# Optimization experiments

Hardware: AMD Instinct MI355X
Metric: run time of the kernel (lower is better)

The kernel has to match this reference:

```python
import jax, jax.numpy as jnp
import numpy as np

EMBED_DIM = 1024
NUM_HEADS = 16
HEAD_DIM = EMBED_DIM // NUM_HEADS
B, N = 4, 2048


def setup_inputs() -> dict:
    key = jax.random.key(0)
    k = jax.random.split(key, 5)
    s = 1.0 / np.sqrt(EMBED_DIM)
    return {
        "x": jax.random.normal(k[0], (B, N, EMBED_DIM), dtype=jnp.float32),
        "W_qkv": jax.random.uniform(k[1], (EMBED_DIM, 3 * EMBED_DIM), jnp.float32, -s, s),
        "b_qkv": jax.random.uniform(k[2], (3 * EMBED_DIM,), jnp.float32, -s, s),
        "W_proj": jax.random.uniform(k[3], (EMBED_DIM, EMBED_DIM), jnp.float32, -s, s),
        "b_proj": jax.random.uniform(k[4], (EMBED_DIM,), jnp.float32, -s, s),
    }


def reference(x, W_qkv, b_qkv, W_proj, b_proj):
    b, n, c = x.shape
    qkv = x @ W_qkv + b_qkv                       # [B,N,3C]
    qkv = qkv.reshape(b, n, 3, NUM_HEADS, HEAD_DIM)
    q = qkv[:, :, 0].transpose(0, 2, 1, 3)        # [B,H,N,D]
    k = qkv[:, :, 1].transpose(0, 2, 1, 3)
    v = qkv[:, :, 2].transpose(0, 2, 1, 3)
    scale = 1.0 / np.sqrt(HEAD_DIM).astype(np.float32)
    scores = jnp.einsum("bhqd,bhkd->bhqk", q, k) * scale
    attn = jax.nn.softmax(scores, axis=-1)
    out = jnp.einsum("bhqk,bhkd->bhqd", attn, v)  # [B,H,N,D]
    out = out.transpose(0, 2, 1, 3).reshape(b, n, c)
    return out @ W_proj + b_proj
```

## Files before the change

### kernel.cpp

```cpp
#include <hip/hip_runtime.h>
#include <math.h>


typedef __bf16 bf16x8 __attribute__((ext_vector_type(8)));
typedef float f32x4 __attribute__((ext_vector_type(4)));

#define EMBED 1024
#define NHEAD 16
#define BATCH 4
#define SEQ 2048
#define M_TOT 8192
#define QKV_N 3072
#define QSCALE 0.18033688011112042f

__device__ __forceinline__ ushort f2bf(float f) {
  union { float f; unsigned u; } x; x.f = f;
  unsigned r = x.u + 0x7FFFu + ((x.u >> 16) & 1u);
  return (ushort)(r >> 16);
}

__device__ __forceinline__ uint cvt2bf(float a, float b) {
#if __has_builtin(__builtin_amdgcn_cvt_pk_bf16_f32)
  typedef __bf16 bf16x2 __attribute__((ext_vector_type(2)));
  union { bf16x2 v; uint u; } c;
  c.v = __builtin_amdgcn_cvt_pk_bf16_f32(a, b);
  return c.u;
#else
  return (uint)f2bf(a) | ((uint)f2bf(b) << 16);
#endif
}

__device__ __forceinline__ float fexp2(float x) {
#if __has_builtin(__builtin_amdgcn_exp2f)
  return __builtin_amdgcn_exp2f(x);
#else
  return exp2f(x);
#endif
}

__device__ __forceinline__ f32x4 mfma16(bf16x8 a, bf16x8 b, f32x4 c) {
  return __builtin_amdgcn_mfma_f32_16x16x32_bf16(a, b, c, 0, 0, 0);
}

__device__ __forceinline__ void gl2lds16(const void* g, void* l) {
  __builtin_amdgcn_global_load_lds(
      (const __attribute__((address_space(1))) unsigned int*)g,
      (__attribute__((address_space(3))) unsigned int*)l, 16, 0, 0);
}

__global__ __launch_bounds__(256) void prep_kernel(
    const float* __restrict__ x, ushort* __restrict__ xb,
    const float* __restrict__ Wqkv, ushort* __restrict__ Wqkv_t,
    const float* __restrict__ Wproj, ushort* __restrict__ Wproj_t) {
  __shared__ float tile[64][65];
  const int bid = blockIdx.x;
  const int t = threadIdx.x;
  if (bid < 8192) {
    int i = (bid * 256 + t) * 4;
    float4 v = *reinterpret_cast<const float4*>(&x[i]);
    uint2 w = {cvt2bf(v.x, v.y), cvt2bf(v.z, v.w)};
    *reinterpret_cast<uint2*>(&xb[i]) = w;
    return;
  }
  const float* in;
  ushort* out;
  int Kd = 1024, Nd, n0, k0;
  if (bid < 8960) {
    int b2 = bid - 8192;
    in = Wqkv; out = Wqkv_t; Nd = 3072;
    n0 = (b2 % 48) * 64; k0 = (b2 / 48) * 64;
  } else {
    int b2 = bid - 8960;
    in = Wproj; out = Wproj_t; Nd = 1024;
    n0 = (b2 % 16) * 64; k0 = (b2 / 16) * 64;
  }
#pragma unroll
  for (int i = 0; i < 16; ++i) {
    int e = t + 256 * i;
    int kr = e >> 6, nc = e & 63;
    tile[kr][nc] = in[(size_t)(k0 + kr) * Nd + n0 + nc];
  }
  __syncthreads();
#pragma unroll
  for (int i = 0; i < 16; ++i) {
    int e = t + 256 * i;
    int nr = e >> 6, kc = e & 63;
    out[(size_t)(n0 + nr) * Kd + k0 + kc] = f2bf(tile[kc][nr]);
  }
}

__global__ __launch_bounds__(512, 4) void gemm_bf16(
    const ushort* __restrict__ A, const ushort* __restrict__ Bt,
    const float* __restrict__ bias, void* __restrict__ Cout,
    ushort* __restrict__ vtgout, int M, int N, int K, int mode) {
  __shared__ ushort As[128 * 64];
  __shared__ ushort Bs[128 * 64];
  const int t = threadIdx.x;
  const int wave = t >> 6, lane = t & 63;
  const int lane15 = lane & 15, quad = lane >> 4;
  const int m0 = blockIdx.y * 128, n0 = blockIdx.x * 128;
  const int wm = (wave >> 2) * 64, wn = (wave & 3) * 32;

  int srow[2], scol[2], sdst[2];
#pragma unroll
  for (int j = 0; j < 2; ++j) {
    int c = (j * 8 + wave) * 64 + lane;
    int row = c >> 3;
    scol[j] = ((c & 7) ^ (row & 7)) * 8;
    srow[j] = row;
    sdst[j] = (j * 8 + wave) * 512;
  }
  const int sw = lane15 & 7;

  f32x4 acc[4][2] = {};

  for (int k0 = 0; k0 < K; k0 += 64) {
#pragma unroll
    for (int j = 0; j < 2; ++j) {
      gl2lds16(&A[(size_t)(m0 + srow[j]) * K + k0 + scol[j]], &As[sdst[j]]);
      gl2lds16(&Bt[(size_t)(n0 + srow[j]) * K + k0 + scol[j]], &Bs[sdst[j]]);
    }
    __syncthreads();

#pragma unroll
    for (int kk = 0; kk < 2; ++kk) {
      bf16x8 af[4], bfr[2];
#pragma unroll
      for (int ms = 0; ms < 4; ++ms)
        af[ms] = *reinterpret_cast<const bf16x8*>(
            &As[(wm + ms * 16 + lane15) * 64 + (((kk * 4 + quad) ^ sw) * 8)]);
#pragma unroll
      for (int ns = 0; ns < 2; ++ns)
        bfr[ns] = *reinterpret_cast<const bf16x8*>(
            &Bs[(wn + ns * 16 + lane15) * 64 + (((kk * 4 + quad) ^ sw) * 8)]);
#pragma unroll
      for (int ms = 0; ms < 4; ++ms)
#pragma unroll
        for (int ns = 0; ns < 2; ++ns)
          acc[ms][ns] = mfma16(af[ms], bfr[ns], acc[ms][ns]);
    }
    __syncthreads();
  }

  if (mode == 0) {
    float* out = (float*)Cout;
#pragma unroll
    for (int ns = 0; ns < 2; ++ns) {
      int col = n0 + wn + ns * 16 + lane15;
      float bv = bias[col];
#pragma unroll
      for (int ms = 0; ms < 4; ++ms)
#pragma unroll
        for (int r = 0; r < 4; ++r) {
          int row = m0 + wm + ms * 16 + quad * 4 + r;
          out[(size_t)row * N + col] = acc[ms][ns][r] + bv;
        }
    }
  } else {
    ushort* qk = (ushort*)Cout;
#pragma unroll
    for (int ns = 0; ns < 2; ++ns) {
      int col = n0 + wn + ns * 16 + lane15;
      float bv = bias[col];
      if (col < 2048) {
        float sc = (col < 1024) ? QSCALE : 1.0f;
#pragma unroll
        for (int ms = 0; ms < 4; ++ms) {
          int row = m0 + wm + ms * 16 + quad * 4;
          uint u01 = cvt2bf((acc[ms][ns][0] + bv) * sc, (acc[ms][ns][1] + bv) * sc);
          uint u23 = cvt2bf((acc[ms][ns][2] + bv) * sc, (acc[ms][ns][3] + bv) * sc);
          qk[(size_t)(row + 0) * 2048 + col] = (ushort)u01;
          qk[(size_t)(row + 1) * 2048 + col] = (ushort)(u01 >> 16);
          qk[(size_t)(row + 2) * 2048 + col] = (ushort)u23;
          qk[(size_t)(row + 3) * 2048 + col] = (ushort)(u23 >> 16);
        }
      } else {
        int dp = col - 2048;
#pragma unroll
        for (int ms = 0; ms < 4; ++ms) {
          int row = m0 + wm + ms * 16 + quad * 4;
          int b = row >> 11, seq = row & 2047;
          uint2 w = {cvt2bf(acc[ms][ns][0] + bv, acc[ms][ns][1] + bv),
                     cvt2bf(acc[ms][ns][2] + bv, acc[ms][ns][3] + bv)};
          *reinterpret_cast<uint2*>(
              &vtgout[((size_t)(b * 1024 + dp) << 11) + seq]) = w;
        }
      }
    }
  }
}

#define QG 2

__global__ __launch_bounds__(256, 4) void attn_kernel(
    const ushort* __restrict__ qk, const ushort* __restrict__ vtg,
    ushort* __restrict__ out) {
  __shared__ ushort Ks[2][4096];
  __shared__ ushort Vt[2][4096];
  __shared__ ushort Ps[4][16 * 64];

  const int t = threadIdx.x;
  const int wave = t >> 6, lane = t & 63;
  const int lane15 = lane & 15, quad = lane >> 4;
  const int bh = blockIdx.x, qg = blockIdx.y;
  const int b = bh >> 4, h = bh & 15;
  const size_t boff = (size_t)b * SEQ * 2048;

  int sdst[2];
  const ushort* kptr[2];
  const ushort* vptr[2];
#pragma unroll
  for (int j = 0; j < 2; ++j) {
    int lg = (j * 4 + wave) * 64 + lane;
    int row = lg >> 3;
    int col = ((lg & 7) ^ (row & 7)) * 8;
    sdst[j] = (j * 4 + wave) * 512;
    kptr[j] = qk + boff + (size_t)row * 2048 + 1024 + h * 64 + col;
    vptr[j] = vtg + ((size_t)(b * 1024 + h * 64 + row) << 11) + col;
  }

  bf16x8 qf[QG][2];
#pragma unroll
  for (int g = 0; g < QG; ++g) {
    size_t qoff = boff +
        (size_t)(qg * (QG * 64) + g * 64 + wave * 16 + lane15) * 2048 + h * 64;
    qf[g][0] = *reinterpret_cast<const bf16x8*>(&qk[qoff + quad * 8]);
    qf[g][1] = *reinterpret_cast<const bf16x8*>(&qk[qoff + 32 + quad * 8]);
  }

  bf16x8 ones;
#pragma unroll
  for (int j = 0; j < 8; ++j) ones[j] = (__bf16)1.0f;

  f32x4 O[QG][4] = {};
  f32x4 lacc[QG] = {};
  const int sw = lane15 & 7;
  ushort* ps = Ps[wave];

#pragma unroll
  for (int j = 0; j < 2; ++j) {
    gl2lds16(kptr[j], &Ks[0][sdst[j]]);
    gl2lds16(vptr[j], &Vt[0][sdst[j]]);
  }
  __syncthreads();

  for (int kt = 0; kt < SEQ / 64; ++kt) {
    const int cur = kt & 1, nxt = cur ^ 1;
    if (kt < SEQ / 64 - 1) {
#pragma unroll
      for (int j = 0; j < 2; ++j) {
        gl2lds16(kptr[j] + (size_t)(kt + 1) * 64 * 2048, &Ks[nxt][sdst[j]]);
        gl2lds16(vptr[j] + (kt + 1) * 64, &Vt[nxt][sdst[j]]);
      }
    }

    bf16x8 kf[4][2], vf[2][4];
#pragma unroll
    for (int nsub = 0; nsub < 4; ++nsub) {
      const int kr = (nsub * 16 + lane15) * 64;
      kf[nsub][0] = *reinterpret_cast<const bf16x8*>(
          &Ks[cur][kr + ((quad ^ sw) * 8)]);
      kf[nsub][1] = *reinterpret_cast<const bf16x8*>(
          &Ks[cur][kr + (((quad + 4) ^ sw) * 8)]);
    }
#pragma unroll
    for (int kk = 0; kk < 2; ++kk)
#pragma unroll
      for (int dsub = 0; dsub < 4; ++dsub) {
        int d = dsub * 16 + lane15;
        vf[kk][dsub] = *reinterpret_cast<const bf16x8*>(
            &Vt[cur][d * 64 + (((kk * 4 + quad) ^ sw) * 8)]);
      }

#pragma unroll
    for (int g = 0; g < QG; ++g) {
      f32x4 st[4];
#pragma unroll
      for (int nsub = 0; nsub < 4; ++nsub) {
        f32x4 a = {-32.0f, -32.0f, -32.0f, -32.0f};
        a = mfma16(kf[nsub][0], qf[g][0], a);
        a = mfma16(kf[nsub][1], qf[g][1], a);
        st[nsub] = a;
      }
#pragma unroll
      for (int nsub = 0; nsub < 4; ++nsub) {
        uint2 w = {cvt2bf(fexp2(st[nsub][0]), fexp2(st[nsub][1])),
                   cvt2bf(fexp2(st[nsub][2]), fexp2(st[nsub][3]))};
        *reinterpret_cast<uint2*>(
            &ps[lane15 * 64 + (((2 * nsub + (quad >> 1)) ^ sw) << 3) +
                ((quad & 1) << 2)]) = w;
      }
#pragma unroll
      for (int kk = 0; kk < 2; ++kk) {
        bf16x8 pf = *reinterpret_cast<const bf16x8*>(
            &ps[lane15 * 64 + (((kk * 4 + quad) ^ sw) << 3)]);
#pragma unroll
        for (int dsub = 0; dsub < 4; ++dsub)
          O[g][dsub] = mfma16(pf, vf[kk][dsub], O[g][dsub]);
        lacc[g] = mfma16(pf, ones, lacc[g]);
      }
    }
    __syncthreads();
  }

#pragma unroll
  for (int g = 0; g < QG; ++g)
#pragma unroll
    for (int r = 0; r < 4; ++r) {
      float linv = __builtin_amdgcn_rcpf(lacc[g][r]);
      size_t rowoff =
          (size_t)(b * SEQ + qg * (QG * 64) + g * 64 + wave * 16 + quad * 4 +
                   r) * EMBED + h * 64;
      uint u01 = cvt2bf(O[g][0][r] * linv, O[g][1][r] * linv);
      uint u23 = cvt2bf(O[g][2][r] * linv, O[g][3][r] * linv);
      out[rowoff + 0 * 16 + lane15] = (ushort)u01;
      out[rowoff + 1 * 16 + lane15] = (ushort)(u01 >> 16);
      out[rowoff + 2 * 16 + lane15] = (ushort)u23;
      out[rowoff + 3 * 16 + lane15] = (ushort)(u23 >> 16);
    }
}

extern "C" void kernel_launch(void* const* d_in, const int* in_sizes, int n_in,
                              void* d_out, int out_size, void* d_ws,
                              size_t ws_size, hipStream_t stream) {
  const float* x = (const float*)d_in[0];
  const float* Wqkv = (const float*)d_in[1];
  const float* bqkv = (const float*)d_in[2];
  const float* Wproj = (const float*)d_in[3];
  const float* bproj = (const float*)d_in[4];
  float* out = (float*)d_out;

  char* ws = (char*)d_ws;
  ushort* Wqkv_t = (ushort*)ws;
  ushort* Wproj_t = (ushort*)(ws + 6291456);
  ushort* qk = (ushort*)(ws + 8388608);
  ushort* vtg = (ushort*)(ws + 41943040);
  ushort* xb = (ushort*)(ws + 58720256);
  ushort* attnout = (ushort*)(ws + 58720256);

  prep_kernel<<<8192 + 768 + 256, 256, 0, stream>>>(
      x, xb, Wqkv, Wqkv_t, Wproj, Wproj_t);
  gemm_bf16<<<dim3(QKV_N / 128, M_TOT / 128), 512, 0, stream>>>(
      xb, Wqkv_t, bqkv, qk, vtg, M_TOT, QKV_N, EMBED, 1);
  attn_kernel<<<dim3(NHEAD * BATCH, SEQ / (QG * 64)), 256, 0, stream>>>(
      qk, vtg, attnout);
  gemm_bf16<<<dim3(EMBED / 128, M_TOT / 128), 512, 0, stream>>>(
      attnout, Wproj_t, bproj, out, nullptr, M_TOT, EMBED, EMBED, 0);
}
```

Measured before the change: 284.5 us.

## Double-buffer GEMM LDS tiles with 32-wide K steps to overlap loads

Restructures the bf16 GEMM main loop to use two 128x32 LDS buffers per operand. The next K-slice is prefetched via direct global-to-LDS loads while MFMAs run on the current slice, and the XOR swizzle is adapted to the 32-element row width. This hides global load latency behind compute and keeps the LDS footprint the same. In exchange there are twice as many iterations and barriers per K, and the tighter swizzle may cause more bank conflicts.

```diff
diff --git a/kernel.cpp b/kernel.cpp
--- a/kernel.cpp
+++ b/kernel.cpp
@@ -93,52 +93,51 @@
     const ushort* __restrict__ A, const ushort* __restrict__ Bt,
     const float* __restrict__ bias, void* __restrict__ Cout,
     ushort* __restrict__ vtgout, int M, int N, int K, int mode) {
-  __shared__ ushort As[128 * 64];
-  __shared__ ushort Bs[128 * 64];
+  __shared__ ushort As[2][128 * 32];
+  __shared__ ushort Bs[2][128 * 32];
   const int t = threadIdx.x;
   const int wave = t >> 6, lane = t & 63;
   const int lane15 = lane & 15, quad = lane >> 4;
   const int m0 = blockIdx.y * 128, n0 = blockIdx.x * 128;
   const int wm = (wave >> 2) * 64, wn = (wave & 3) * 32;
 
-  int srow[2], scol[2], sdst[2];
-#pragma unroll
-  for (int j = 0; j < 2; ++j) {
-    int c = (j * 8 + wave) * 64 + lane;
-    int row = c >> 3;
-    scol[j] = ((c & 7) ^ (row & 7)) * 8;
-    srow[j] = row;
-    sdst[j] = (j * 8 + wave) * 512;
-  }
-  const int sw = lane15 & 7;
+  const int srow = t >> 2;
+  const int scol = ((t & 3) ^ ((srow >> 1) & 3)) * 8;
+  const int sdst = wave * 512;
+  const ushort* ap = &A[(size_t)(m0 + srow) * K + scol];
+  const ushort* bp = &Bt[(size_t)(n0 + srow) * K + scol];
+
+  const int sw2 = (lane15 >> 1) & 3;
 
   f32x4 acc[4][2] = {};
 
-  for (int k0 = 0; k0 < K; k0 += 64) {
-#pragma unroll
-    for (int j = 0; j < 2; ++j) {
-      gl2lds16(&A[(size_t)(m0 + srow[j]) * K + k0 + scol[j]], &As[sdst[j]]);
-      gl2lds16(&Bt[(size_t)(n0 + srow[j]) * K + k0 + scol[j]], &Bs[sdst[j]]);
-    }
-    __syncthreads();
-
-#pragma unroll
-    for (int kk = 0; kk < 2; ++kk) {
-      bf16x8 af[4], bfr[2];
-#pragma unroll
-      for (int ms = 0; ms < 4; ++ms)
-        af[ms] = *reinterpret_cast<const bf16x8*>(
-            &As[(wm + ms * 16 + lane15) * 64 + (((kk * 4 + quad) ^ sw) * 8)]);
+  const int NIT = K >> 5;
+  gl2lds16(ap, &As[0][sdst]);
+  gl2lds16(bp, &Bs[0][sdst]);
+  __syncthreads();
+
+  for (int kt = 0; kt < NIT; ++kt) {
+    const int cur = kt & 1, nxt = cur ^ 1;
+    if (kt < NIT - 1) {
+      gl2lds16(ap + (kt + 1) * 32, &As[nxt][sdst]);
+      gl2lds16(bp + (kt + 1) * 32, &Bs[nxt][sdst]);
+    }
+
+    bf16x8 af[4], bfr[2];
+#pragma unroll
+    for (int ms = 0; ms < 4; ++ms)
+      af[ms] = *reinterpret_cast<const bf16x8*>(
+          &As[cur][(wm + ms * 16 + lane15) * 32 + ((quad ^ sw2) * 8)]);
+#pragma unroll
+    for (int ns = 0; ns < 2; ++ns)
+      bfr[ns] = *reinterpret_cast<const bf16x8*>(
+          &Bs[cur][(wn + ns * 16 + lane15) * 32 + ((quad ^ sw2) * 8)]);
+#pragma unroll
+    for (int ms = 0; ms < 4; ++ms)
 #pragma unroll
       for (int ns = 0; ns < 2; ++ns)
-        bfr[ns] = *reinterpret_cast<const bf16x8*>(
-            &Bs[(wn + ns * 16 + lane15) * 64 + (((kk * 4 + quad) ^ sw) * 8)]);
-#pragma unroll
-      for (int ms = 0; ms < 4; ++ms)
-#pragma unroll
-        for (int ns = 0; ns < 2; ++ns)
-          acc[ms][ns] = mfma16(af[ms], bfr[ns], acc[ms][ns]);
-    }
+        acc[ms][ns] = mfma16(af[ms], bfr[ns], acc[ms][ns]);
+
     __syncthreads();
   }
 
```

Measured after the change: 293.5 us. +3.2%, slower.

## Double-buffer LDS tiles in bf16 GEMM to overlap global loads with MFMA

Applied to the files above, without the earlier changes.

The GEMM kernel now keeps two LDS buffers for the A and B tiles. It prefetches the next K-tile through direct global-to-LDS loads while computing MFMAs on the current tile, using one barrier per iteration instead of two. Global row pointers are also precomputed once. This aims to hide memory latency behind compute, at the cost of doubling LDS use per block, which may lower occupancy.

```diff
diff --git a/kernel.cpp b/kernel.cpp
--- a/kernel.cpp
+++ b/kernel.cpp
@@ -93,34 +93,47 @@
     const ushort* __restrict__ A, const ushort* __restrict__ Bt,
     const float* __restrict__ bias, void* __restrict__ Cout,
     ushort* __restrict__ vtgout, int M, int N, int K, int mode) {
-  __shared__ ushort As[128 * 64];
-  __shared__ ushort Bs[128 * 64];
+  __shared__ ushort As[2][128 * 64];
+  __shared__ ushort Bs[2][128 * 64];
   const int t = threadIdx.x;
   const int wave = t >> 6, lane = t & 63;
   const int lane15 = lane & 15, quad = lane >> 4;
   const int m0 = blockIdx.y * 128, n0 = blockIdx.x * 128;
   const int wm = (wave >> 2) * 64, wn = (wave & 3) * 32;
 
-  int srow[2], scol[2], sdst[2];
+  int sdst[2];
+  const ushort* ap[2];
+  const ushort* bp[2];
 #pragma unroll
   for (int j = 0; j < 2; ++j) {
     int c = (j * 8 + wave) * 64 + lane;
     int row = c >> 3;
-    scol[j] = ((c & 7) ^ (row & 7)) * 8;
-    srow[j] = row;
+    int scol = ((c & 7) ^ (row & 7)) * 8;
     sdst[j] = (j * 8 + wave) * 512;
+    ap[j] = &A[(size_t)(m0 + row) * K + scol];
+    bp[j] = &Bt[(size_t)(n0 + row) * K + scol];
   }
   const int sw = lane15 & 7;
 
   f32x4 acc[4][2] = {};
 
-  for (int k0 = 0; k0 < K; k0 += 64) {
-#pragma unroll
-    for (int j = 0; j < 2; ++j) {
-      gl2lds16(&A[(size_t)(m0 + srow[j]) * K + k0 + scol[j]], &As[sdst[j]]);
-      gl2lds16(&Bt[(size_t)(n0 + srow[j]) * K + k0 + scol[j]], &Bs[sdst[j]]);
-    }
-    __syncthreads();
+  const int NIT = K >> 6;
+#pragma unroll
+  for (int j = 0; j < 2; ++j) {
+    gl2lds16(ap[j], &As[0][sdst[j]]);
+    gl2lds16(bp[j], &Bs[0][sdst[j]]);
+  }
+  __syncthreads();
+
+  for (int kt = 0; kt < NIT; ++kt) {
+    const int cur = kt & 1, nxt = cur ^ 1;
+    if (kt < NIT - 1) {
+#pragma unroll
+      for (int j = 0; j < 2; ++j) {
+        gl2lds16(ap[j] + (kt + 1) * 64, &As[nxt][sdst[j]]);
+        gl2lds16(bp[j] + (kt + 1) * 64, &Bs[nxt][sdst[j]]);
+      }
+    }
 
 #pragma unroll
     for (int kk = 0; kk < 2; ++kk) {
@@ -128,17 +141,18 @@
 #pragma unroll
       for (int ms = 0; ms < 4; ++ms)
         af[ms] = *reinterpret_cast<const bf16x8*>(
-            &As[(wm + ms * 16 + lane15) * 64 + (((kk * 4 + quad) ^ sw) * 8)]);
+            &As[cur][(wm + ms * 16 + lane15) * 64 + (((kk * 4 + quad) ^ sw) * 8)]);
 #pragma unroll
       for (int ns = 0; ns < 2; ++ns)
         bfr[ns] = *reinterpret_cast<const bf16x8*>(
-            &Bs[(wn + ns * 16 + lane15) * 64 + (((kk * 4 + quad) ^ sw) * 8)]);
+            &Bs[cur][(wn + ns * 16 + lane15) * 64 + (((kk * 4 + quad) ^ sw) * 8)]);
 #pragma unroll
       for (int ms = 0; ms < 4; ++ms)
 #pragma unroll
         for (int ns = 0; ns < 2; ++ns)
           acc[ms][ns] = mfma16(af[ms], bfr[ns], acc[ms][ns]);
     }
+
     __syncthreads();
   }
 
```

Result: no change. 285.0 us (+0.2%).
